# Kernel tuning notes

Measured on AMD Instinct MI355X. Metric: run time of the kernel, lower is better.

Reference implementation:

```python
import jax, jax.numpy as jnp
import numpy as np

DROPOUT_P = 0.5
NUM_NODES = 50000


def _gcn_layer(x, W, b, src, dst, ew, num_nodes):
    # support = x @ W ; out = A_hat @ support + b, with A_hat given as edge list
    h = x @ W                               # [N, out_dim]
    msg = h[src] * ew[:, None]              # [E, out_dim]
    agg = jax.ops.segment_sum(msg, dst, num_segments=num_nodes)  # [N, out_dim]
    return agg + b


def setup_inputs() -> dict:
    key = jax.random.key(0)
    ks = jax.random.split(key, 8)
    N, E, F_in, H, C = NUM_NODES, 800000, 512, 128, 64
    x = jax.random.normal(ks[0], (N, F_in), dtype=jnp.float32)
    edge_weight = jax.random.uniform(ks[1], (E,), dtype=jnp.float32)
    W1 = jax.random.normal(ks[2], (F_in, H), dtype=jnp.float32) * (1.0 / np.sqrt(F_in))
    b1 = jax.random.normal(ks[3], (H,), dtype=jnp.float32) * 0.01
    W2 = jax.random.normal(ks[4], (H, C), dtype=jnp.float32) * (1.0 / np.sqrt(H))
    b2 = jax.random.normal(ks[5], (C,), dtype=jnp.float32) * 0.01
    drop_mask = jax.random.uniform(ks[6], (N, H), dtype=jnp.float32)
    edge_index = jax.random.randint(ks[7], (2, E), 0, N, dtype=jnp.int32)
    return {"x": x, "edge_weight": edge_weight, "W1": W1, "b1": b1,
            "W2": W2, "b2": b2, "drop_mask": drop_mask, "edge_index": edge_index}


def reference(x, edge_weight, W1, b1, W2, b2, drop_mask, edge_index):
    src, dst = edge_index[0], edge_index[1]
    h = _gcn_layer(x, W1, b1, src, dst, edge_weight, NUM_NODES)
    h = jax.nn.relu(h)
    # deterministic inverted dropout using precomputed uniform mask
    keep = (drop_mask >= DROPOUT_P).astype(h.dtype)
    h = h * keep / (1.0 - DROPOUT_P)
    h = _gcn_layer(h, W2, b2, src, dst, edge_weight, NUM_NODES)
    return jax.nn.log_softmax(h, axis=1)
```

## Files before the change

### kernel.cpp

```cpp
#include <hip/hip_runtime.h>
#include <cstdint>
#include <cstddef>

constexpr int FIN = 512;
constexpr int HD  = 128;
constexpr int CD  = 64;

typedef __attribute__((ext_vector_type(8))) short short8;
typedef __attribute__((ext_vector_type(4))) float f32x4;

__device__ inline unsigned short f2bf(float f) {
  unsigned int u = __float_as_uint(f);
  u += 0x7fffu + ((u >> 16) & 1u);
  return (unsigned short)(u >> 16);
}
__device__ inline float bf_lo(unsigned int v) { return __uint_as_float(v << 16); }
__device__ inline float bf_hi(unsigned int v) { return __uint_as_float(v & 0xffff0000u); }


__global__ __launch_bounds__(256) void hist_kernel(const int* __restrict__ dst, int E,
                                                   int* __restrict__ cnt) {
  int i = blockIdx.x * 256 + threadIdx.x;
  if (i < E) atomicAdd(&cnt[dst[i]], 1);
}

__global__ __launch_bounds__(256) void scan_a(const int* __restrict__ cnt,
                                              int* __restrict__ bs, int n) {
  __shared__ int sh[256];
  int t = threadIdx.x;
  int base = blockIdx.x * 2048;
  int s = 0;
#pragma unroll
  for (int j = 0; j < 8; ++j) {
    int idx = base + j * 256 + t;
    if (idx < n) s += cnt[idx];
  }
  sh[t] = s;
  __syncthreads();
  for (int o = 128; o > 0; o >>= 1) {
    if (t < o) sh[t] += sh[t + o];
    __syncthreads();
  }
  if (t == 0) bs[blockIdx.x] = sh[0];
}

__global__ __launch_bounds__(64) void scan_b(const int* __restrict__ bs,
                                             int* __restrict__ bo, int nb) {
  int t = threadIdx.x;
  int v = (t < nb) ? bs[t] : 0;
  int own = v;
#pragma unroll
  for (int o = 1; o < 64; o <<= 1) {
    int u = __shfl_up(v, o, 64);
    if (t >= o) v += u;
  }
  if (t < nb) bo[t] = v - own;
}

__global__ __launch_bounds__(256) void scan_c(const int* __restrict__ cnt,
                                              const int* __restrict__ bo,
                                              int* __restrict__ off,
                                              int* __restrict__ cur, int n) {
  __shared__ int sh[256];
  int t = threadIdx.x;
  int base = blockIdx.x * 2048 + t * 8;
  int v[8];
  int local = 0;
#pragma unroll
  for (int j = 0; j < 8; ++j) {
    v[j] = (base + j < n) ? cnt[base + j] : 0;
    local += v[j];
  }
  sh[t] = local;
  __syncthreads();
  for (int o = 1; o < 256; o <<= 1) {
    int u = (t >= o) ? sh[t - o] : 0;
    __syncthreads();
    sh[t] += u;
    __syncthreads();
  }
  int run = sh[t] - local + bo[blockIdx.x];
#pragma unroll
  for (int j = 0; j < 8; ++j) {
    if (base + j < n) { off[base + j] = run; cur[base + j] = run; }
    run += v[j];
  }
}

__global__ __launch_bounds__(256) void scatter_kernel(const int* __restrict__ src,
                                                      const int* __restrict__ dst,
                                                      const float* __restrict__ ew, int E,
                                                      int* __restrict__ cur,
                                                      int2* __restrict__ sew) {
  int i = blockIdx.x * 256 + threadIdx.x;
  if (i < E) {
    int d = dst[i];
    int p = atomicAdd(&cur[d], 1);
    sew[p] = make_int2(src[i], __float_as_int(ew[i]));
  }
}


__global__ __launch_bounds__(256) void w1t_prep(const float* __restrict__ W1,
                                                unsigned short* __restrict__ w1t) {
  int idx = blockIdx.x * 256 + threadIdx.x;
  int k = idx >> 7;
  int n = idx & 127;
  w1t[(size_t)n * FIN + k] = f2bf(W1[idx]);
}


__global__ __launch_bounds__(256) void gemm1_mfma(const float* __restrict__ x,
                                                  const unsigned short* __restrict__ w1t,
                                                  unsigned short* __restrict__ h1b, int M) {
  __shared__ unsigned short As[64][40];
  __shared__ unsigned short Bs[128][40];
  const int t    = threadIdx.x;
  const int wave = t >> 6;
  const int lane = t & 63;
  const int l15  = lane & 15;
  const int quad = lane >> 4;
  const int m0   = blockIdx.x * 64;

  const int ra = t >> 2;
  const int ka = (t & 3) * 8;
  const int rb = t >> 1;
  const int kb = (t & 1) * 16;

  const bool aok = (m0 + ra) < M;
  const float* xrow = x + (size_t)(m0 + ra) * FIN + ka;
  const unsigned short* brow = w1t + (size_t)rb * FIN + kb;

  f32x4 acc[8];
#pragma unroll
  for (int i = 0; i < 8; ++i) acc[i] = (f32x4)0.f;

  for (int k0 = 0; k0 < FIN; k0 += 32) {
    float4 f0 = make_float4(0.f, 0.f, 0.f, 0.f);
    float4 f1 = f0;
    if (aok) {
      f0 = *(const float4*)(xrow + k0);
      f1 = *(const float4*)(xrow + k0 + 4);
    }
    uint4 b0 = *(const uint4*)(brow + k0);
    uint4 b1 = *(const uint4*)(brow + k0 + 8);
    __syncthreads();
    unsigned short tmp[8];
    tmp[0] = f2bf(f0.x); tmp[1] = f2bf(f0.y); tmp[2] = f2bf(f0.z); tmp[3] = f2bf(f0.w);
    tmp[4] = f2bf(f1.x); tmp[5] = f2bf(f1.y); tmp[6] = f2bf(f1.z); tmp[7] = f2bf(f1.w);
    *(uint4*)&As[ra][ka] = *(const uint4*)tmp;
    *(uint4*)&Bs[rb][kb] = b0;
    *(uint4*)&Bs[rb][kb + 8] = b1;
    __syncthreads();
    short8 af = *(const short8*)&As[wave * 16 + l15][quad * 8];
#pragma unroll
    for (int nt = 0; nt < 8; ++nt) {
      short8 bf = *(const short8*)&Bs[nt * 16 + l15][quad * 8];
      acc[nt] = __builtin_amdgcn_mfma_f32_16x16x32_bf16(af, bf, acc[nt], 0, 0, 0);
    }
  }
  const int row0 = m0 + wave * 16 + quad * 4;
#pragma unroll
  for (int r = 0; r < 4; ++r) {
    int row = row0 + r;
    if (row < M) {
      unsigned short* orow = h1b + (size_t)row * HD + l15;
#pragma unroll
      for (int nt = 0; nt < 8; ++nt) orow[nt * 16] = f2bf(acc[nt][r]);
    }
  }
}


__global__ __launch_bounds__(256) void agg1_kernel(const unsigned int* __restrict__ h1b,
                                                   const float* __restrict__ b1,
                                                   const float* __restrict__ dm,
                                                   const int* __restrict__ off,
                                                   const int* __restrict__ cnt,
                                                   const int2* __restrict__ sew,
                                                   float* __restrict__ h, int N) {
  const int wave = threadIdx.x >> 6;
  const int lane = threadIdx.x & 63;
  const int node = blockIdx.x * 4 + wave;
  if (node >= N) return;
  const int start = off[node];
  const int deg   = cnt[node];
  const int2* ep  = sew + start;

  float a0 = 0.f, a1 = 0.f, c0 = 0.f, c1 = 0.f;
  int e = 0;
  for (; e + 4 <= deg; e += 4) {
    int2 p0 = ep[e + 0];
    int2 p1 = ep[e + 1];
    int2 p2 = ep[e + 2];
    int2 p3 = ep[e + 3];
    unsigned int v0 = h1b[(size_t)p0.x * 64 + lane];
    unsigned int v1 = h1b[(size_t)p1.x * 64 + lane];
    unsigned int v2 = h1b[(size_t)p2.x * 64 + lane];
    unsigned int v3 = h1b[(size_t)p3.x * 64 + lane];
    float w0 = __int_as_float(p0.y), w1 = __int_as_float(p1.y);
    float w2 = __int_as_float(p2.y), w3 = __int_as_float(p3.y);
    a0 = fmaf(bf_lo(v0), w0, a0); a1 = fmaf(bf_hi(v0), w0, a1);
    c0 = fmaf(bf_lo(v1), w1, c0); c1 = fmaf(bf_hi(v1), w1, c1);
    a0 = fmaf(bf_lo(v2), w2, a0); a1 = fmaf(bf_hi(v2), w2, a1);
    c0 = fmaf(bf_lo(v3), w3, c0); c1 = fmaf(bf_hi(v3), w3, c1);
  }
  for (; e < deg; ++e) {
    int2 p = ep[e];
    unsigned int v = h1b[(size_t)p.x * 64 + lane];
    float w = __int_as_float(p.y);
    a0 = fmaf(bf_lo(v), w, a0); a1 = fmaf(bf_hi(v), w, a1);
  }
  a0 += c0; a1 += c1;

  const int f0 = lane * 2;
  float2 bb = *(const float2*)(b1 + f0);
  float2 dd = *(const float2*)(dm + (size_t)node * HD + f0);
  float r0 = fmaxf(a0 + bb.x, 0.f) * ((dd.x >= 0.5f) ? 2.0f : 0.0f);
  float r1 = fmaxf(a1 + bb.y, 0.f) * ((dd.y >= 0.5f) ? 2.0f : 0.0f);
  *(float2*)(h + (size_t)node * HD + f0) = make_float2(r0, r1);
}


__global__ __launch_bounds__(256) void gemm2_kernel(const float* __restrict__ h,
                                                    const float* __restrict__ W2,
                                                    float* __restrict__ h2, int M) {
  __shared__ float As[16][68];
  __shared__ float Bs[16][68];
  const int t    = threadIdx.x;
  const int m0   = blockIdx.x * 64;
  const int tx   = t & 15;
  const int ty   = t >> 4;
  const int lrow = t >> 2;
  const int lk4  = (t & 3) << 2;
  const int grow = m0 + lrow;
  const bool rowok = grow < M;
  const float* hrow = h + (size_t)grow * HD;

  float acc[4][4];
#pragma unroll
  for (int i = 0; i < 4; ++i)
#pragma unroll
    for (int j = 0; j < 4; ++j) acc[i][j] = 0.f;

  const int i0 = t * 4;
  const int r0i = i0 >> 6, c0i = i0 & 63;

  for (int k0 = 0; k0 < HD; k0 += 16) {
    float4 av = make_float4(0.f, 0.f, 0.f, 0.f);
    if (rowok) av = *(const float4*)(hrow + k0 + lk4);
    float4 bv0 = *(const float4*)(W2 + (size_t)(k0 + r0i) * CD + c0i);
    __syncthreads();
    As[lk4 + 0][lrow] = av.x;
    As[lk4 + 1][lrow] = av.y;
    As[lk4 + 2][lrow] = av.z;
    As[lk4 + 3][lrow] = av.w;
    *(float4*)&Bs[r0i][c0i] = bv0;
    __syncthreads();
#pragma unroll
    for (int kk = 0; kk < 16; ++kk) {
      float4 a = *(const float4*)&As[kk][ty << 2];
      float4 b = *(const float4*)&Bs[kk][tx << 2];
      float am[4] = {a.x, a.y, a.z, a.w};
      float bn[4] = {b.x, b.y, b.z, b.w};
#pragma unroll
      for (int i = 0; i < 4; ++i)
#pragma unroll
        for (int j = 0; j < 4; ++j) acc[i][j] = fmaf(am[i], bn[j], acc[i][j]);
    }
  }
#pragma unroll
  for (int i = 0; i < 4; ++i) {
    int r = m0 + (ty << 2) + i;
    if (r < M) {
      float4 o0 = {acc[i][0], acc[i][1], acc[i][2], acc[i][3]};
      *(float4*)(h2 + (size_t)r * CD + (tx << 2)) = o0;
    }
  }
}


__global__ __launch_bounds__(256) void agg2_kernel(const float* __restrict__ h2,
                                                   const float* __restrict__ b2,
                                                   const int* __restrict__ off,
                                                   const int* __restrict__ cnt,
                                                   const int2* __restrict__ sew,
                                                   float* __restrict__ out, int N) {
  const int wave = threadIdx.x >> 6;
  const int c    = threadIdx.x & 63;
  const int node = blockIdx.x * 4 + wave;
  if (node >= N) return;
  const int start = off[node];
  const int deg   = cnt[node];
  const int2* ep  = sew + start;

  float acc = b2[c], acc2 = 0.f;
  int e = 0;
  for (; e + 4 <= deg; e += 4) {
    int2 p0 = ep[e + 0];
    int2 p1 = ep[e + 1];
    int2 p2 = ep[e + 2];
    int2 p3 = ep[e + 3];
    float v0 = h2[(size_t)p0.x * CD + c];
    float v1 = h2[(size_t)p1.x * CD + c];
    float v2 = h2[(size_t)p2.x * CD + c];
    float v3 = h2[(size_t)p3.x * CD + c];
    acc  = fmaf(v0, __int_as_float(p0.y), acc);
    acc2 = fmaf(v1, __int_as_float(p1.y), acc2);
    acc  = fmaf(v2, __int_as_float(p2.y), acc);
    acc2 = fmaf(v3, __int_as_float(p3.y), acc2);
  }
  for (; e < deg; ++e) {
    int2 p = ep[e];
    acc = fmaf(h2[(size_t)p.x * CD + c], __int_as_float(p.y), acc);
  }
  acc += acc2;

  float m = acc;
#pragma unroll
  for (int o = 32; o > 0; o >>= 1) m = fmaxf(m, __shfl_xor(m, o, 64));
  float ex = __expf(acc - m);
  float ssum = ex;
#pragma unroll
  for (int o = 32; o > 0; o >>= 1) ssum += __shfl_xor(ssum, o, 64);
  out[(size_t)node * CD + c] = (acc - m) - __logf(ssum);
}


extern "C" void kernel_launch(void* const* d_in, const int* in_sizes, int n_in,
                              void* d_out, int out_size, void* d_ws, size_t ws_size,
                              hipStream_t stream) {
  const float* x  = (const float*)d_in[0];
  const float* ew = (const float*)d_in[1];
  const float* W1 = (const float*)d_in[2];
  const float* b1 = (const float*)d_in[3];
  const float* W2 = (const float*)d_in[4];
  const float* b2 = (const float*)d_in[5];
  const float* dm = (const float*)d_in[6];
  const int*   ei = (const int*)d_in[7];
  float* out = (float*)d_out;

  const int E = in_sizes[1];
  const int N = in_sizes[6] / HD;
  const int* srcp = ei;
  const int* dstp = ei + E;
  const int nb = (N + 2047) / 2048;

  uint8_t* w = (uint8_t*)d_ws;
  size_t o = 0;
  auto alloc = [&](size_t bytes) -> void* {
    void* p = w + o;
    o = (o + bytes + 255) & ~(size_t)255;
    return p;
  };
  int*   off  = (int*)alloc((size_t)N * 4);
  int*   cnt  = (int*)alloc((size_t)N * 4);
  int*   cur  = (int*)alloc((size_t)N * 4);
  int2*  sew  = (int2*)alloc((size_t)E * 8);
  unsigned short* h1b = (unsigned short*)alloc((size_t)N * HD * 2);
  float* h    = (float*)alloc((size_t)N * HD * 4);
  float* h2   = (float*)alloc((size_t)N * CD * 4);
  unsigned short* w1t = (unsigned short*)alloc((size_t)FIN * HD * 2);
  int*   bsum = (int*)alloc((size_t)nb * 4);
  int*   boff = (int*)alloc((size_t)nb * 4);

  hipMemsetAsync(cnt, 0, (size_t)N * 4, stream);
  w1t_prep<<<(FIN * HD) / 256, 256, 0, stream>>>(W1, w1t);
  hist_kernel<<<(E + 255) / 256, 256, 0, stream>>>(dstp, E, cnt);
  scan_a<<<nb, 256, 0, stream>>>(cnt, bsum, N);
  scan_b<<<1, 64, 0, stream>>>(bsum, boff, nb);
  scan_c<<<nb, 256, 0, stream>>>(cnt, boff, off, cur, N);
  scatter_kernel<<<(E + 255) / 256, 256, 0, stream>>>(srcp, dstp, ew, E, cur, sew);
  gemm1_mfma<<<(N + 63) / 64, 256, 0, stream>>>(x, w1t, h1b, N);
  agg1_kernel<<<(N + 3) / 4, 256, 0, stream>>>((const unsigned int*)h1b, b1, dm, off, cnt, sew, h, N);
  gemm2_kernel<<<(N + 63) / 64, 256, 0, stream>>>(h, W2, h2, N);
  agg2_kernel<<<(N + 3) / 4, 256, 0, stream>>>(h2, b2, off, cnt, sew, out, N);
}
```

Before: 397.4 us.

## Move second GEMM to bf16 MFMA and store hidden activations in bf16

Replaces the fp32 SIMT second GEMM with a bf16 MFMA kernel, fed by a W2 transpose added to the weight-prep kernel. The relu/dropout output and the layer-2 features are now stored as bf16, halving the bytes written and the bytes gathered per edge in the second aggregation. The first GEMM tile grows from 64 to 128 rows per block, so each wave does two M sub-tiles and each B tile loaded into shared memory is reused twice. The cost is extra bf16 rounding error in the layer-2 inputs and outputs, and fewer blocks in both GEMMs.

```diff
diff --git a/kernel.cpp b/kernel.cpp
--- a/kernel.cpp
+++ b/kernel.cpp
@@ -16,6 +16,7 @@
 }
 __device__ inline float bf_lo(unsigned int v) { return __uint_as_float(v << 16); }
 __device__ inline float bf_hi(unsigned int v) { return __uint_as_float(v & 0xffff0000u); }
+__device__ inline float bf1(unsigned short v) { return __uint_as_float((unsigned int)v << 16); }
 
 
 __global__ __launch_bounds__(256) void hist_kernel(const int* __restrict__ dst, int E,
@@ -101,72 +102,90 @@
 }
 
 
-__global__ __launch_bounds__(256) void w1t_prep(const float* __restrict__ W1,
-                                                unsigned short* __restrict__ w1t) {
+__global__ __launch_bounds__(256) void wprep(const float* __restrict__ W1,
+                                             const float* __restrict__ W2,
+                                             unsigned short* __restrict__ w1t,
+                                             unsigned short* __restrict__ w2t) {
   int idx = blockIdx.x * 256 + threadIdx.x;
-  int k = idx >> 7;
-  int n = idx & 127;
-  w1t[(size_t)n * FIN + k] = f2bf(W1[idx]);
+  if (idx < FIN * HD) {
+    int k = idx >> 7, n = idx & 127;
+    w1t[(size_t)n * FIN + k] = f2bf(W1[idx]);
+  } else {
+    int j = idx - FIN * HD;
+    if (j < HD * CD) {
+      int k = j >> 6, n = j & 63;
+      w2t[(size_t)n * HD + k] = f2bf(W2[j]);
+    }
+  }
 }
 
 
 __global__ __launch_bounds__(256) void gemm1_mfma(const float* __restrict__ x,
                                                   const unsigned short* __restrict__ w1t,
                                                   unsigned short* __restrict__ h1b, int M) {
-  __shared__ unsigned short As[64][40];
+  __shared__ unsigned short As[128][40];
   __shared__ unsigned short Bs[128][40];
   const int t    = threadIdx.x;
   const int wave = t >> 6;
   const int lane = t & 63;
   const int l15  = lane & 15;
   const int quad = lane >> 4;
-  const int m0   = blockIdx.x * 64;
-
-  const int ra = t >> 2;
-  const int ka = (t & 3) * 8;
-  const int rb = t >> 1;
-  const int kb = (t & 1) * 16;
-
-  const bool aok = (m0 + ra) < M;
-  const float* xrow = x + (size_t)(m0 + ra) * FIN + ka;
-  const unsigned short* brow = w1t + (size_t)rb * FIN + kb;
-
-  f32x4 acc[8];
-#pragma unroll
-  for (int i = 0; i < 8; ++i) acc[i] = (f32x4)0.f;
+  const int m0   = blockIdx.x * 128;
+
+  const int sr = t >> 1;
+  const int sk = (t & 1) * 16;
+
+  const bool aok = (m0 + sr) < M;
+  const float* xrow = x + (size_t)(m0 + sr) * FIN + sk;
+  const unsigned short* brow = w1t + (size_t)sr * FIN + sk;
+
+  f32x4 acc[2][8];
+#pragma unroll
+  for (int i = 0; i < 2; ++i)
+#pragma unroll
+    for (int j = 0; j < 8; ++j) acc[i][j] = (f32x4)0.f;
 
   for (int k0 = 0; k0 < FIN; k0 += 32) {
-    float4 f0 = make_float4(0.f, 0.f, 0.f, 0.f);
-    float4 f1 = f0;
+    float4 a0 = make_float4(0.f, 0.f, 0.f, 0.f), a1 = a0, a2 = a0, a3 = a0;
     if (aok) {
-      f0 = *(const float4*)(xrow + k0);
-      f1 = *(const float4*)(xrow + k0 + 4);
+      a0 = *(const float4*)(xrow + k0);
+      a1 = *(const float4*)(xrow + k0 + 4);
+      a2 = *(const float4*)(xrow + k0 + 8);
+      a3 = *(const float4*)(xrow + k0 + 12);
     }
     uint4 b0 = *(const uint4*)(brow + k0);
     uint4 b1 = *(const uint4*)(brow + k0 + 8);
     __syncthreads();
-    unsigned short tmp[8];
-    tmp[0] = f2bf(f0.x); tmp[1] = f2bf(f0.y); tmp[2] = f2bf(f0.z); tmp[3] = f2bf(f0.w);
-    tmp[4] = f2bf(f1.x); tmp[5] = f2bf(f1.y); tmp[6] = f2bf(f1.z); tmp[7] = f2bf(f1.w);
-    *(uint4*)&As[ra][ka] = *(const uint4*)tmp;
-    *(uint4*)&Bs[rb][kb] = b0;
-    *(uint4*)&Bs[rb][kb + 8] = b1;
-    __syncthreads();
-    short8 af = *(const short8*)&As[wave * 16 + l15][quad * 8];
+    unsigned short tmp[16];
+    tmp[0]  = f2bf(a0.x); tmp[1]  = f2bf(a0.y); tmp[2]  = f2bf(a0.z); tmp[3]  = f2bf(a0.w);
+    tmp[4]  = f2bf(a1.x); tmp[5]  = f2bf(a1.y); tmp[6]  = f2bf(a1.z); tmp[7]  = f2bf(a1.w);
+    tmp[8]  = f2bf(a2.x); tmp[9]  = f2bf(a2.y); tmp[10] = f2bf(a2.z); tmp[11] = f2bf(a2.w);
+    tmp[12] = f2bf(a3.x); tmp[13] = f2bf(a3.y); tmp[14] = f2bf(a3.z); tmp[15] = f2bf(a3.w);
+    *(uint4*)&As[sr][sk]     = ((const uint4*)tmp)[0];
+    *(uint4*)&As[sr][sk + 8] = ((const uint4*)tmp)[1];
+    *(uint4*)&Bs[sr][sk]     = b0;
+    *(uint4*)&Bs[sr][sk + 8] = b1;
+    __syncthreads();
+    short8 af0 = *(const short8*)&As[wave * 32 + l15][quad * 8];
+    short8 af1 = *(const short8*)&As[wave * 32 + 16 + l15][quad * 8];
 #pragma unroll
     for (int nt = 0; nt < 8; ++nt) {
       short8 bf = *(const short8*)&Bs[nt * 16 + l15][quad * 8];
-      acc[nt] = __builtin_amdgcn_mfma_f32_16x16x32_bf16(af, bf, acc[nt], 0, 0, 0);
-    }
-  }
-  const int row0 = m0 + wave * 16 + quad * 4;
-#pragma unroll
-  for (int r = 0; r < 4; ++r) {
-    int row = row0 + r;
-    if (row < M) {
-      unsigned short* orow = h1b + (size_t)row * HD + l15;
-#pragma unroll
-      for (int nt = 0; nt < 8; ++nt) orow[nt * 16] = f2bf(acc[nt][r]);
+      acc[0][nt] = __builtin_amdgcn_mfma_f32_16x16x32_bf16(af0, bf, acc[0][nt], 0, 0, 0);
+      acc[1][nt] = __builtin_amdgcn_mfma_f32_16x16x32_bf16(af1, bf, acc[1][nt], 0, 0, 0);
+    }
+  }
+#pragma unroll
+  for (int mt = 0; mt < 2; ++mt) {
+    const int row0 = m0 + wave * 32 + mt * 16 + quad * 4;
+#pragma unroll
+    for (int r = 0; r < 4; ++r) {
+      int row = row0 + r;
+      if (row < M) {
+        unsigned short* orow = h1b + (size_t)row * HD + l15;
+#pragma unroll
+        for (int nt = 0; nt < 8; ++nt) orow[nt * 16] = f2bf(acc[mt][nt][r]);
+      }
     }
   }
 }
@@ -178,7 +197,7 @@
                                                    const int* __restrict__ off,
                                                    const int* __restrict__ cnt,
                                                    const int2* __restrict__ sew,
-                                                   float* __restrict__ h, int N) {
+                                                   unsigned int* __restrict__ hbf, int N) {
   const int wave = threadIdx.x >> 6;
   const int lane = threadIdx.x & 63;
   const int node = blockIdx.x * 4 + wave;
@@ -218,69 +237,75 @@
   float2 dd = *(const float2*)(dm + (size_t)node * HD + f0);
   float r0 = fmaxf(a0 + bb.x, 0.f) * ((dd.x >= 0.5f) ? 2.0f : 0.0f);
   float r1 = fmaxf(a1 + bb.y, 0.f) * ((dd.y >= 0.5f) ? 2.0f : 0.0f);
-  *(float2*)(h + (size_t)node * HD + f0) = make_float2(r0, r1);
-}
-
-
-__global__ __launch_bounds__(256) void gemm2_kernel(const float* __restrict__ h,
-                                                    const float* __restrict__ W2,
-                                                    float* __restrict__ h2, int M) {
-  __shared__ float As[16][68];
-  __shared__ float Bs[16][68];
+  hbf[(size_t)node * 64 + lane] = (unsigned int)f2bf(r0) | ((unsigned int)f2bf(r1) << 16);
+}
+
+
+__global__ __launch_bounds__(256) void gemm2_mfma(const unsigned short* __restrict__ hbf,
+                                                  const unsigned short* __restrict__ w2t,
+                                                  unsigned short* __restrict__ h2b, int M) {
+  __shared__ unsigned short As[128][40];
+  __shared__ unsigned short Bs[64][40];
   const int t    = threadIdx.x;
-  const int m0   = blockIdx.x * 64;
-  const int tx   = t & 15;
-  const int ty   = t >> 4;
-  const int lrow = t >> 2;
-  const int lk4  = (t & 3) << 2;
-  const int grow = m0 + lrow;
-  const bool rowok = grow < M;
-  const float* hrow = h + (size_t)grow * HD;
-
-  float acc[4][4];
-#pragma unroll
-  for (int i = 0; i < 4; ++i)
-#pragma unroll
-    for (int j = 0; j < 4; ++j) acc[i][j] = 0.f;
-
-  const int i0 = t * 4;
-  const int r0i = i0 >> 6, c0i = i0 & 63;
-
-  for (int k0 = 0; k0 < HD; k0 += 16) {
-    float4 av = make_float4(0.f, 0.f, 0.f, 0.f);
-    if (rowok) av = *(const float4*)(hrow + k0 + lk4);
-    float4 bv0 = *(const float4*)(W2 + (size_t)(k0 + r0i) * CD + c0i);
-    __syncthreads();
-    As[lk4 + 0][lrow] = av.x;
-    As[lk4 + 1][lrow] = av.y;
-    As[lk4 + 2][lrow] = av.z;
-    As[lk4 + 3][lrow] = av.w;
-    *(float4*)&Bs[r0i][c0i] = bv0;
-    __syncthreads();
-#pragma unroll
-    for (int kk = 0; kk < 16; ++kk) {
-      float4 a = *(const float4*)&As[kk][ty << 2];
-      float4 b = *(const float4*)&Bs[kk][tx << 2];
-      float am[4] = {a.x, a.y, a.z, a.w};
-      float bn[4] = {b.x, b.y, b.z, b.w};
-#pragma unroll
-      for (int i = 0; i < 4; ++i)
-#pragma unroll
-        for (int j = 0; j < 4; ++j) acc[i][j] = fmaf(am[i], bn[j], acc[i][j]);
-    }
-  }
-#pragma unroll
-  for (int i = 0; i < 4; ++i) {
-    int r = m0 + (ty << 2) + i;
-    if (r < M) {
-      float4 o0 = {acc[i][0], acc[i][1], acc[i][2], acc[i][3]};
-      *(float4*)(h2 + (size_t)r * CD + (tx << 2)) = o0;
-    }
-  }
-}
-
-
-__global__ __launch_bounds__(256) void agg2_kernel(const float* __restrict__ h2,
+  const int wave = t >> 6;
+  const int lane = t & 63;
+  const int l15  = lane & 15;
+  const int quad = lane >> 4;
+  const int m0   = blockIdx.x * 128;
+
+  const int sr = t >> 1;
+  const int sk = (t & 1) * 16;
+  const int rb = t >> 2;
+  const int kb = (t & 3) * 8;
+
+  const bool aok = (m0 + sr) < M;
+  const unsigned short* arow = hbf + (size_t)(m0 + sr) * HD + sk;
+  const unsigned short* brow = w2t + (size_t)rb * HD + kb;
+
+  f32x4 acc[2][4];
+#pragma unroll
+  for (int i = 0; i < 2; ++i)
+#pragma unroll
+    for (int j = 0; j < 4; ++j) acc[i][j] = (f32x4)0.f;
+
+  for (int k0 = 0; k0 < HD; k0 += 32) {
+    uint4 av0 = make_uint4(0, 0, 0, 0), av1 = av0;
+    if (aok) {
+      av0 = *(const uint4*)(arow + k0);
+      av1 = *(const uint4*)(arow + k0 + 8);
+    }
+    uint4 bv = *(const uint4*)(brow + k0);
+    __syncthreads();
+    *(uint4*)&As[sr][sk]     = av0;
+    *(uint4*)&As[sr][sk + 8] = av1;
+    *(uint4*)&Bs[rb][kb]     = bv;
+    __syncthreads();
+    short8 af0 = *(const short8*)&As[wave * 32 + l15][quad * 8];
+    short8 af1 = *(const short8*)&As[wave * 32 + 16 + l15][quad * 8];
+#pragma unroll
+    for (int nt = 0; nt < 4; ++nt) {
+      short8 bf = *(const short8*)&Bs[nt * 16 + l15][quad * 8];
+      acc[0][nt] = __builtin_amdgcn_mfma_f32_16x16x32_bf16(af0, bf, acc[0][nt], 0, 0, 0);
+      acc[1][nt] = __builtin_amdgcn_mfma_f32_16x16x32_bf16(af1, bf, acc[1][nt], 0, 0, 0);
+    }
+  }
+#pragma unroll
+  for (int mt = 0; mt < 2; ++mt) {
+    const int row0 = m0 + wave * 32 + mt * 16 + quad * 4;
+#pragma unroll
+    for (int r = 0; r < 4; ++r) {
+      int row = row0 + r;
+      if (row < M) {
+        unsigned short* orow = h2b + (size_t)row * CD + l15;
+#pragma unroll
+        for (int nt = 0; nt < 4; ++nt) orow[nt * 16] = f2bf(acc[mt][nt][r]);
+      }
+    }
+  }
+}
+
+
+__global__ __launch_bounds__(256) void agg2_kernel(const unsigned short* __restrict__ h2b,
                                                    const float* __restrict__ b2,
                                                    const int* __restrict__ off,
                                                    const int* __restrict__ cnt,
@@ -301,10 +326,10 @@
     int2 p1 = ep[e + 1];
     int2 p2 = ep[e + 2];
     int2 p3 = ep[e + 3];
-    float v0 = h2[(size_t)p0.x * CD + c];
-    float v1 = h2[(size_t)p1.x * CD + c];
-    float v2 = h2[(size_t)p2.x * CD + c];
-    float v3 = h2[(size_t)p3.x * CD + c];
+    float v0 = bf1(h2b[(size_t)p0.x * CD + c]);
+    float v1 = bf1(h2b[(size_t)p1.x * CD + c]);
+    float v2 = bf1(h2b[(size_t)p2.x * CD + c]);
+    float v3 = bf1(h2b[(size_t)p3.x * CD + c]);
     acc  = fmaf(v0, __int_as_float(p0.y), acc);
     acc2 = fmaf(v1, __int_as_float(p1.y), acc2);
     acc  = fmaf(v2, __int_as_float(p2.y), acc);
@@ -312,7 +337,7 @@
   }
   for (; e < deg; ++e) {
     int2 p = ep[e];
-    acc = fmaf(h2[(size_t)p.x * CD + c], __int_as_float(p.y), acc);
+    acc = fmaf(bf1(h2b[(size_t)p.x * CD + c]), __int_as_float(p.y), acc);
   }
   acc += acc2;
 
@@ -358,21 +383,22 @@
   int*   cur  = (int*)alloc((size_t)N * 4);
   int2*  sew  = (int2*)alloc((size_t)E * 8);
   unsigned short* h1b = (unsigned short*)alloc((size_t)N * HD * 2);
-  float* h    = (float*)alloc((size_t)N * HD * 4);
-  float* h2   = (float*)alloc((size_t)N * CD * 4);
+  unsigned int*   hbf = (unsigned int*)alloc((size_t)N * HD * 2);
+  unsigned short* h2b = (unsigned short*)alloc((size_t)N * CD * 2);
   unsigned short* w1t = (unsigned short*)alloc((size_t)FIN * HD * 2);
+  unsigned short* w2t = (unsigned short*)alloc((size_t)HD * CD * 2);
   int*   bsum = (int*)alloc((size_t)nb * 4);
   int*   boff = (int*)alloc((size_t)nb * 4);
 
   hipMemsetAsync(cnt, 0, (size_t)N * 4, stream);
-  w1t_prep<<<(FIN * HD) / 256, 256, 0, stream>>>(W1, w1t);
+  wprep<<<(FIN * HD + HD * CD + 255) / 256, 256, 0, stream>>>(W1, W2, w1t, w2t);
   hist_kernel<<<(E + 255) / 256, 256, 0, stream>>>(dstp, E, cnt);
   scan_a<<<nb, 256, 0, stream>>>(cnt, bsum, N);
   scan_b<<<1, 64, 0, stream>>>(bsum, boff, nb);
   scan_c<<<nb, 256, 0, stream>>>(cnt, boff, off, cur, N);
   scatter_kernel<<<(E + 255) / 256, 256, 0, stream>>>(srcp, dstp, ew, E, cur, sew);
-  gemm1_mfma<<<(N + 63) / 64, 256, 0, stream>>>(x, w1t, h1b, N);
-  agg1_kernel<<<(N + 3) / 4, 256, 0, stream>>>((const unsigned int*)h1b, b1, dm, off, cnt, sew, h, N);
-  gemm2_kernel<<<(N + 63) / 64, 256, 0, stream>>>(h, W2, h2, N);
-  agg2_kernel<<<(N + 3) / 4, 256, 0, stream>>>(h2, b2, off, cnt, sew, out, N);
-}
+  gemm1_mfma<<<(N + 127) / 128, 256, 0, stream>>>(x, w1t, h1b, N);
+  agg1_kernel<<<(N + 3) / 4, 256, 0, stream>>>((const unsigned int*)h1b, b1, dm, off, cnt, sew, hbf, N);
+  gemm2_mfma<<<(N + 127) / 128, 256, 0, stream>>>((const unsigned short*)hbf, w2t, h2b, N);
+  agg2_kernel<<<(N + 3) / 4, 256, 0, stream>>>(h2b, b2, off, cnt, sew, out, N);
+}
```

Result: faster. 372.2 us (-6.3%).
